# Performance work log

Hardware: AMD Instinct MI355X
Metric: run time of the kernel (lower is better)

## Reference

```python
import jax, jax.numpy as jnp
import numpy as np

N = 50000          # nodes
E = 800000         # directed edges (before self-loops)
F_IN = 256
HIDS = 32
HEADS = 8
N_CLASSES = 40
NEG_SLOPE = 0.2    # PyG GATConv default leaky_relu slope


def setup_inputs() -> dict:
    key = jax.random.key(0)
    ks = jax.random.split(key, 10)
    x = jax.random.normal(ks[0], (N, F_IN), dtype=jnp.float32)
    edge_index = jax.random.randint(ks[1], (2, E), 0, N, dtype=jnp.int32)
    # conv1: F_IN -> HIDS per head, HEADS heads, concat=True
    W1 = jax.random.normal(ks[2], (F_IN, HEADS * HIDS), dtype=jnp.float32) * (1.0 / np.sqrt(F_IN))
    a1_src = jax.random.normal(ks[3], (HEADS, HIDS), dtype=jnp.float32) * 0.1
    a1_dst = jax.random.normal(ks[4], (HEADS, HIDS), dtype=jnp.float32) * 0.1
    b1 = jnp.zeros((HEADS * HIDS,), dtype=jnp.float32)
    # conv2: HEADS*HIDS -> N_CLASSES, 1 head, concat=False
    W2 = jax.random.normal(ks[5], (HEADS * HIDS, N_CLASSES), dtype=jnp.float32) * (1.0 / np.sqrt(HEADS * HIDS))
    a2_src = jax.random.normal(ks[6], (1, N_CLASSES), dtype=jnp.float32) * 0.1
    a2_dst = jax.random.normal(ks[7], (1, N_CLASSES), dtype=jnp.float32) * 0.1
    b2 = jnp.zeros((N_CLASSES,), dtype=jnp.float32)
    return {"x": x, "edge_index": edge_index, "W1": W1, "a1_src": a1_src,
            "a1_dst": a1_dst, "b1": b1, "W2": W2, "a2_src": a2_src,
            "a2_dst": a2_dst, "b2": b2}


def _gat_conv(x, src, dst, W, a_src, a_dst, bias, heads, concat):
    n = x.shape[0]
    c = W.shape[1] // heads
    xw = (x @ W).reshape(n, heads, c)                       # [N,H,C]
    alpha_s = jnp.einsum('nhc,hc->nh', xw, a_src)           # [N,H]
    alpha_d = jnp.einsum('nhc,hc->nh', xw, a_dst)
    e = alpha_s[src] + alpha_d[dst]                         # [Etot,H]
    e = jnp.where(e >= 0, e, NEG_SLOPE * e)                 # leaky_relu
    # segment softmax over incoming edges of each destination node
    m = jax.ops.segment_max(e, dst, num_segments=n)         # [N,H]
    ex = jnp.exp(e - m[dst])
    denom = jax.ops.segment_sum(ex, dst, num_segments=n)    # [N,H]
    alpha = ex / denom[dst]                                 # [Etot,H]
    out = jax.ops.segment_sum(alpha[:, :, None] * xw[src], dst, num_segments=n)  # [N,H,C]
    if concat:
        out = out.reshape(n, heads * c)
    else:
        out = out.mean(axis=1)
    return out + bias


def reference(x, edge_index, W1, a1_src, a1_dst, b1, W2, a2_src, a2_dst, b2):
    n = x.shape[0]
    # add self-loops (PyG GATConv default)
    loop = jnp.arange(n, dtype=edge_index.dtype)
    src = jnp.concatenate([edge_index[0], loop])
    dst = jnp.concatenate([edge_index[1], loop])
    # dropout(p=0.6) layers are identity in eval mode
    h = _gat_conv(x, src, dst, W1, a1_src, a1_dst, b1, HEADS, True)
    h = jax.nn.elu(h)
    out = _gat_conv(h, src, dst, W2, a2_src, a2_dst, b2, 1, False)
    return out
```

## Files before the change

kernel.cpp:

```cpp
#include <hip/hip_runtime.h>
#include <hip/hip_bf16.h>

#define NNODES 50000
#define NPAD   50048
#define NEDGES 800000
#define ETOT   (NEDGES + NNODES)
#define FIN    256
#define HIDS   32
#define HEADS  8
#define NCLS   40
#define NEG    0.2f

#define SCAN_B 256
#define NSCB   ((NNODES + SCAN_B - 1) / SCAN_B)
#define NTILE1 ((NNODES + 63) / 64)

typedef __attribute__((ext_vector_type(8))) short bf16x8;
typedef __attribute__((ext_vector_type(4))) float f32x4;

__device__ __forceinline__ ushort f2bf(float f) {
  unsigned u = __float_as_uint(f);
  unsigned r = (u + 0x7fffu + ((u >> 16) & 1u)) >> 16;
  return (ushort)r;
}
__device__ __forceinline__ float bf2f(ushort u) {
  return __uint_as_float(((unsigned)u) << 16);
}
__device__ __forceinline__ float bflo(unsigned u) { return __uint_as_float(u << 16); }
__device__ __forceinline__ float bfhi(unsigned u) { return __uint_as_float(u & 0xffff0000u); }

__global__ __launch_bounds__(256) void prep_k(
    const float* __restrict__ W1, const float* __restrict__ W2,
    const float* __restrict__ a1src, const float* __restrict__ a1dst,
    const float* __restrict__ a2src, const float* __restrict__ a2dst,
    ushort* __restrict__ w1t, ushort* __restrict__ w2t,
    int* __restrict__ cnt, ushort* __restrict__ hb) {
  int b = blockIdx.x, t = threadIdx.x;
  if (b < 256) {
    int k = b, n = t;
    w1t[(size_t)n * 256 + k] = f2bf(W1[(size_t)k * 256 + n]);
  } else if (b < 272) {
    int j = b - 256, k = t;
    const float* av = (j < 8) ? (a1src + j * 32) : (a1dst + (j - 8) * 32);
    int nb = (j < 8) ? j * 32 : (j - 8) * 32;
    float s = 0.f;
#pragma unroll
    for (int c = 0; c < 32; ++c) s += W1[(size_t)k * 256 + nb + c] * av[c];
    w1t[(size_t)(256 + j) * 256 + k] = f2bf(s);
  } else if (b < 320) {
    w1t[(size_t)b * 256 + t] = 0;
  } else if (b < 384) {
    int n = b - 320, k = t;
    ushort v;
    if (n < NCLS) {
      v = f2bf(W2[(size_t)k * NCLS + n]);
    } else if (n == 40) {
      float s = 0.f;
#pragma unroll
      for (int c = 0; c < NCLS; ++c) s += W2[(size_t)k * NCLS + c] * a2src[c];
      v = f2bf(s);
    } else if (n == 41) {
      float s = 0.f;
#pragma unroll
      for (int c = 0; c < NCLS; ++c) s += W2[(size_t)k * NCLS + c] * a2dst[c];
      v = f2bf(s);
    } else {
      v = 0;
    }
    w2t[(size_t)n * 256 + k] = v;
  } else if (b < 580) {
    int i = (b - 384) * 256 + t;
    if (i < NNODES) cnt[i] = 0;
  } else {
    int r = NNODES + (b - 580);
    hb[(size_t)r * 256 + t] = 0;
  }
}

__global__ __launch_bounds__(256) void gemm1_mfma(
    const float* __restrict__ x, const ushort* __restrict__ w1t,
    ushort* __restrict__ xw1s, float* __restrict__ a1s, float* __restrict__ a1d) {
  __shared__ ushort As[64 * 40];
  __shared__ ushort Bs[320 * 40];
  const int tid = threadIdx.x;
  const int m0 = blockIdx.x * 64;
  const int w = tid >> 6, l = tid & 63, lr = l & 15, lq = l >> 4;
  f32x4 acc[4][5];
#pragma unroll
  for (int i = 0; i < 4; ++i)
#pragma unroll
    for (int j = 0; j < 5; ++j) acc[i][j] = (f32x4)0.f;

  for (int k0 = 0; k0 < 256; k0 += 32) {
    {
      int row = tid >> 2, kg = (tid & 3) * 8;
      int gr = m0 + row;
      bf16x8 av;
      if (gr < NNODES) {
        const float4* xp = (const float4*)(x + (size_t)gr * 256 + k0 + kg);
        float4 p0 = xp[0], p1 = xp[1];
        av[0] = (short)f2bf(p0.x); av[1] = (short)f2bf(p0.y);
        av[2] = (short)f2bf(p0.z); av[3] = (short)f2bf(p0.w);
        av[4] = (short)f2bf(p1.x); av[5] = (short)f2bf(p1.y);
        av[6] = (short)f2bf(p1.z); av[7] = (short)f2bf(p1.w);
      } else {
        av = (bf16x8)0;
      }
      *(bf16x8*)&As[row * 40 + kg] = av;
    }
#pragma unroll
    for (int p = 0; p < 5; ++p) {
      int idx = tid + p * 256;
      int n = idx >> 2, kg = (idx & 3) * 8;
      *(bf16x8*)&Bs[n * 40 + kg] = *(const bf16x8*)(w1t + (size_t)n * 256 + k0 + kg);
    }
    __syncthreads();
    bf16x8 af[4], bfr[5];
#pragma unroll
    for (int mt = 0; mt < 4; ++mt)
      af[mt] = *(const bf16x8*)&As[(mt * 16 + lr) * 40 + lq * 8];
#pragma unroll
    for (int nt = 0; nt < 5; ++nt) {
      int tile = nt * 4 + w;
      bfr[nt] = *(const bf16x8*)&Bs[(tile * 16 + lr) * 40 + lq * 8];
    }
#pragma unroll
    for (int mt = 0; mt < 4; ++mt)
#pragma unroll
      for (int nt = 0; nt < 5; ++nt)
        acc[mt][nt] = __builtin_amdgcn_mfma_f32_16x16x32_bf16(af[mt], bfr[nt], acc[mt][nt], 0, 0, 0);
    __syncthreads();
  }
#pragma unroll
  for (int mt = 0; mt < 4; ++mt)
#pragma unroll
    for (int nt = 0; nt < 5; ++nt) {
      int tile = nt * 4 + w;
      if (tile < 16) {
        int colc = tile * 16 + lr;
        int s = colc >> 5, c = colc & 31;
#pragma unroll
        for (int r = 0; r < 4; ++r) {
          int row = m0 + mt * 16 + lq * 4 + r;
          xw1s[((size_t)s * NPAD + row) * 32 + c] = f2bf(acc[mt][nt][r]);
        }
      } else if (tile == 16) {
#pragma unroll
        for (int r = 0; r < 4; ++r) {
          int row = m0 + mt * 16 + lq * 4 + r;
          if (lr < 8) a1s[(size_t)row * 8 + lr] = acc[mt][nt][r];
          else        a1d[(size_t)row * 8 + (lr - 8)] = acc[mt][nt][r];
        }
      }
    }
}

__global__ __launch_bounds__(256) void gemm2_mfma(
    const ushort* __restrict__ hb, const ushort* __restrict__ w2t,
    ushort* __restrict__ xw2b, float* __restrict__ a2s, float* __restrict__ a2d) {
  const int tid = threadIdx.x;
  const int w = tid >> 6, l = tid & 63, lr = l & 15, lq = l >> 4;
  const int row0 = blockIdx.x * 64 + w * 16;
  f32x4 acc[3];
#pragma unroll
  for (int i = 0; i < 3; ++i) acc[i] = (f32x4)0.f;
#pragma unroll
  for (int ks = 0; ks < 8; ++ks) {
    int k0 = ks * 32;
    bf16x8 af = *(const bf16x8*)(hb + (size_t)(row0 + lr) * 256 + k0 + lq * 8);
#pragma unroll
    for (int nt = 0; nt < 3; ++nt) {
      bf16x8 bfr = *(const bf16x8*)(w2t + (size_t)(nt * 16 + lr) * 256 + k0 + lq * 8);
      acc[nt] = __builtin_amdgcn_mfma_f32_16x16x32_bf16(af, bfr, acc[nt], 0, 0, 0);
    }
  }
#pragma unroll
  for (int nt = 0; nt < 3; ++nt) {
    int colc = nt * 16 + lr;
#pragma unroll
    for (int r = 0; r < 4; ++r) {
      int row = row0 + lq * 4 + r;
      if (colc < NCLS)      xw2b[(size_t)row * 40 + colc] = f2bf(acc[nt][r]);
      else if (colc == 40)  a2s[row] = acc[nt][r];
      else if (colc == 41)  a2d[row] = acc[nt][r];
    }
  }
}

__global__ __launch_bounds__(256) void hist_k(const int* __restrict__ dstA, int* __restrict__ cnt) {
  int e = blockIdx.x * 256 + threadIdx.x;
  if (e >= ETOT) return;
  int d = (e < NEDGES) ? dstA[e] : (e - NEDGES);
  atomicAdd(&cnt[d], 1);
}

__global__ __launch_bounds__(SCAN_B) void scan1_k(const int* __restrict__ deg,
                                                  int* __restrict__ row_ptr,
                                                  int* __restrict__ bsum) {
  __shared__ int sm[SCAN_B];
  int b = blockIdx.x, t = threadIdx.x;
  int idx = b * SCAN_B + t;
  int v = (idx < NNODES) ? deg[idx] : 0;
  sm[t] = v;
  __syncthreads();
#pragma unroll
  for (int off = 1; off < SCAN_B; off <<= 1) {
    int u = (t >= off) ? sm[t - off] : 0;
    __syncthreads();
    sm[t] += u;
    __syncthreads();
  }
  if (idx < NNODES) row_ptr[idx + 1] = sm[t];
  if (t == SCAN_B - 1) bsum[b] = sm[t];
}

__global__ __launch_bounds__(256) void scan2_k(int* __restrict__ bsum) {
  __shared__ int sm[256];
  int t = threadIdx.x;
  sm[t] = (t < NSCB) ? bsum[t] : 0;
  __syncthreads();
#pragma unroll
  for (int off = 1; off < 256; off <<= 1) {
    int u = (t >= off) ? sm[t - off] : 0;
    __syncthreads();
    sm[t] += u;
    __syncthreads();
  }
  if (t < NSCB) bsum[t] = (t > 0) ? sm[t - 1] : 0;
}

__global__ __launch_bounds__(SCAN_B) void scan3_k(const int* __restrict__ bsum,
                                                  int* __restrict__ row_ptr) {
  int b = blockIdx.x, t = threadIdx.x;
  int idx = b * SCAN_B + t;
  if (idx < NNODES) row_ptr[idx + 1] += bsum[b];
  if (b == 0 && t == 0) row_ptr[0] = 0;
}

__global__ __launch_bounds__(256) void scatter_k(const int* __restrict__ srcA, const int* __restrict__ dstA,
                                                 const int* __restrict__ row_ptr, int* __restrict__ cnt,
                                                 int* __restrict__ col, int* __restrict__ edst) {
  int e = blockIdx.x * 256 + threadIdx.x;
  if (e >= ETOT) return;
  int s, d;
  if (e < NEDGES) { s = srcA[e]; d = dstA[e]; }
  else { s = d = e - NEDGES; }
  int old = atomicSub(&cnt[d], 1);
  int pos = row_ptr[d] + old - 1;
  col[pos] = s;
  edst[pos] = d;
}

__global__ __launch_bounds__(256) void ew_k(
    const float* __restrict__ a1s, const float* __restrict__ a1d,
    const int* __restrict__ col, const int* __restrict__ edst,
    float* __restrict__ ew) {
  int pos = blockIdx.x * 256 + threadIdx.x;
  if (pos >= ETOT) return;
  int src = col[pos], dst = edst[pos];
  const float4* sp = (const float4*)(a1s + (size_t)src * 8);
  const float4* dp = (const float4*)(a1d + (size_t)dst * 8);
  float4 s0 = sp[0], s1 = sp[1];
  float4 d0 = dp[0], d1 = dp[1];
  float e[8] = {s0.x + d0.x, s0.y + d0.y, s0.z + d0.z, s0.w + d0.w,
                s1.x + d1.x, s1.y + d1.y, s1.z + d1.z, s1.w + d1.w};
#pragma unroll
  for (int h = 0; h < 8; ++h) {
    float v = e[h];
    v = fmaxf(v, 0.f) + NEG * fminf(v, 0.f);
    ew[(size_t)h * ETOT + pos] = __expf(v);
  }
}

__global__ __launch_bounds__(256) void agg1_k(
    const ushort* __restrict__ xw1s, const float* __restrict__ ew,
    const int* __restrict__ row_ptr, const int* __restrict__ col,
    const float* __restrict__ b1, ushort* __restrict__ hb) {
  const int b = blockIdx.x;
  const int s = b & 7;
  const int t = threadIdx.x;
  const int node = (b >> 3) * 64 + (t >> 2);
  const int q = t & 3;
  if (node >= NNODES) return;
  const ushort* xs = xw1s + (size_t)s * NPAD * 32 + q * 8;
  const float* ws = ew + (size_t)s * ETOT;
  int i = row_ptr[node];
  const int end = row_ptr[node + 1];
  float den = 0.f;
  float c0 = 0.f, c1 = 0.f, c2 = 0.f, c3 = 0.f, c4 = 0.f, c5 = 0.f, c6 = 0.f, c7 = 0.f;
  for (; i + 4 <= end; i += 4) {
    int s0 = col[i], s1 = col[i + 1], s2 = col[i + 2], s3 = col[i + 3];
    float w0 = ws[i], w1 = ws[i + 1], w2 = ws[i + 2], w3 = ws[i + 3];
    uint4 u0 = *(const uint4*)(xs + (size_t)s0 * 32);
    uint4 u1 = *(const uint4*)(xs + (size_t)s1 * 32);
    uint4 u2 = *(const uint4*)(xs + (size_t)s2 * 32);
    uint4 u3 = *(const uint4*)(xs + (size_t)s3 * 32);
    den += (w0 + w1) + (w2 + w3);
    c0 += w0 * bflo(u0.x) + w1 * bflo(u1.x) + w2 * bflo(u2.x) + w3 * bflo(u3.x);
    c1 += w0 * bfhi(u0.x) + w1 * bfhi(u1.x) + w2 * bfhi(u2.x) + w3 * bfhi(u3.x);
    c2 += w0 * bflo(u0.y) + w1 * bflo(u1.y) + w2 * bflo(u2.y) + w3 * bflo(u3.y);
    c3 += w0 * bfhi(u0.y) + w1 * bfhi(u1.y) + w2 * bfhi(u2.y) + w3 * bfhi(u3.y);
    c4 += w0 * bflo(u0.z) + w1 * bflo(u1.z) + w2 * bflo(u2.z) + w3 * bflo(u3.z);
    c5 += w0 * bfhi(u0.z) + w1 * bfhi(u1.z) + w2 * bfhi(u2.z) + w3 * bfhi(u3.z);
    c6 += w0 * bflo(u0.w) + w1 * bflo(u1.w) + w2 * bflo(u2.w) + w3 * bflo(u3.w);
    c7 += w0 * bfhi(u0.w) + w1 * bfhi(u1.w) + w2 * bfhi(u2.w) + w3 * bfhi(u3.w);
  }
  for (; i < end; ++i) {
    int s0 = col[i];
    float w0 = ws[i];
    uint4 u0 = *(const uint4*)(xs + (size_t)s0 * 32);
    den += w0;
    c0 += w0 * bflo(u0.x); c1 += w0 * bfhi(u0.x);
    c2 += w0 * bflo(u0.y); c3 += w0 * bfhi(u0.y);
    c4 += w0 * bflo(u0.z); c5 += w0 * bfhi(u0.z);
    c6 += w0 * bflo(u0.w); c7 += w0 * bfhi(u0.w);
  }
  const float inv = 1.f / den;
  const float4 bv0 = *reinterpret_cast<const float4*>(b1 + s * 32 + q * 8);
  const float4 bv1 = *reinterpret_cast<const float4*>(b1 + s * 32 + q * 8 + 4);
  float o[8];
  o[0] = c0 * inv + bv0.x; o[1] = c1 * inv + bv0.y;
  o[2] = c2 * inv + bv0.z; o[3] = c3 * inv + bv0.w;
  o[4] = c4 * inv + bv1.x; o[5] = c5 * inv + bv1.y;
  o[6] = c6 * inv + bv1.z; o[7] = c7 * inv + bv1.w;
  uint4 pk;
  unsigned r[4];
#pragma unroll
  for (int p = 0; p < 4; ++p) {
    float a = o[2 * p],     va = (a > 0.f) ? a : expm1f(a);
    float c = o[2 * p + 1], vc = (c > 0.f) ? c : expm1f(c);
    r[p] = (unsigned)f2bf(va) | ((unsigned)f2bf(vc) << 16);
  }
  pk.x = r[0]; pk.y = r[1]; pk.z = r[2]; pk.w = r[3];
  *(uint4*)(hb + (size_t)node * 256 + s * 32 + q * 8) = pk;
}

__global__ __launch_bounds__(256) void agg2_k(
    const ushort* __restrict__ xw2b, const float* __restrict__ a2s, const float* __restrict__ a2d,
    const int* __restrict__ row_ptr, const int* __restrict__ col,
    const float* __restrict__ b2, float* __restrict__ out, int n) {
  int wid = (blockIdx.x * 256 + threadIdx.x) >> 6;
  if (wid >= n) return;
  int lane = threadIdx.x & 63;
  int beg = row_ptr[wid], end = row_ptr[wid + 1];
  float ad = a2d[wid];
  float denom = 0.f, acc = 0.f;
  int i = beg;
  for (; i + 4 <= end; i += 4) {
    int s0 = col[i], s1 = col[i + 1], s2 = col[i + 2], s3 = col[i + 3];
    float e0 = a2s[s0] + ad;
    float e1 = a2s[s1] + ad;
    float e2 = a2s[s2] + ad;
    float e3 = a2s[s3] + ad;
    float w0 = __expf(fmaxf(e0, 0.f) + NEG * fminf(e0, 0.f));
    float w1 = __expf(fmaxf(e1, 0.f) + NEG * fminf(e1, 0.f));
    float w2 = __expf(fmaxf(e2, 0.f) + NEG * fminf(e2, 0.f));
    float w3 = __expf(fmaxf(e3, 0.f) + NEG * fminf(e3, 0.f));
    float x0 = 0.f, x1 = 0.f, x2 = 0.f, x3 = 0.f;
    if (lane < NCLS) {
      x0 = bf2f(xw2b[(size_t)s0 * 40 + lane]);
      x1 = bf2f(xw2b[(size_t)s1 * 40 + lane]);
      x2 = bf2f(xw2b[(size_t)s2 * 40 + lane]);
      x3 = bf2f(xw2b[(size_t)s3 * 40 + lane]);
    }
    denom += (w0 + w1) + (w2 + w3);
    acc += w0 * x0 + w1 * x1 + w2 * x2 + w3 * x3;
  }
  for (; i < end; ++i) {
    int s = col[i];
    float e = a2s[s] + ad;
    float w = __expf(fmaxf(e, 0.f) + NEG * fminf(e, 0.f));
    denom += w;
    if (lane < NCLS) acc += w * bf2f(xw2b[(size_t)s * 40 + lane]);
  }
  if (lane < NCLS) out[(size_t)wid * 40 + lane] = acc / denom + b2[lane];
}

extern "C" void kernel_launch(void* const* d_in, const int* in_sizes, int n_in,
                              void* d_out, int out_size, void* d_ws, size_t ws_size,
                              hipStream_t stream) {
  const float* x     = (const float*)d_in[0];
  const int*   ei    = (const int*)d_in[1];
  const float* W1    = (const float*)d_in[2];
  const float* a1src = (const float*)d_in[3];
  const float* a1dst = (const float*)d_in[4];
  const float* b1    = (const float*)d_in[5];
  const float* W2    = (const float*)d_in[6];
  const float* a2src = (const float*)d_in[7];
  const float* a2dst = (const float*)d_in[8];
  const float* b2    = (const float*)d_in[9];
  float* out = (float*)d_out;

  const int* srcA = ei;
  const int* dstA = ei + NEDGES;

  ushort* w1t  = (ushort*)d_ws;
  ushort* w2t  = w1t + (size_t)320 * 256;
  ushort* xw1s = w2t + (size_t)64 * 256;
  ushort* hb   = xw1s + (size_t)NPAD * 256;
  ushort* xw2b = hb + (size_t)NPAD * 256;
  float* a1s   = (float*)(xw2b + (size_t)NPAD * 40);
  float* a1d   = a1s + (size_t)NPAD * 8;
  float* a2s   = a1d + (size_t)NPAD * 8;
  float* a2d   = a2s + NPAD;
  float* ew    = a2d + NPAD;
  int* row_ptr = (int*)(ew + (size_t)8 * ETOT);
  int* cnt     = row_ptr + (NNODES + 1);
  int* col     = cnt + NNODES;
  int* edst    = col + ETOT;
  int* bsum    = edst + ETOT;

  prep_k<<<628, 256, 0, stream>>>(W1, W2, a1src, a1dst, a2src, a2dst, w1t, w2t, cnt, hb);

  gemm1_mfma<<<NPAD / 64, 256, 0, stream>>>(x, w1t, xw1s, a1s, a1d);

  hist_k<<<(ETOT + 255) / 256, 256, 0, stream>>>(dstA, cnt);
  scan1_k<<<NSCB, SCAN_B, 0, stream>>>(cnt, row_ptr, bsum);
  scan2_k<<<1, 256, 0, stream>>>(bsum);
  scan3_k<<<NSCB, SCAN_B, 0, stream>>>(bsum, row_ptr);
  scatter_k<<<(ETOT + 255) / 256, 256, 0, stream>>>(srcA, dstA, row_ptr, cnt, col, edst);

  ew_k<<<(ETOT + 255) / 256, 256, 0, stream>>>(a1s, a1d, col, edst, ew);

  agg1_k<<<NTILE1 * 8, 256, 0, stream>>>(xw1s, ew, row_ptr, col, b1, hb);

  gemm2_mfma<<<NPAD / 64, 256, 0, stream>>>(hb, w2t, xw2b, a2s, a2d);

  agg2_k<<<(NNODES + 3) / 4, 256, 0, stream>>>(xw2b, a2s, a2d, row_ptr, col, b2, out, NNODES);
}
```

Measured before the change: 263.8 us.

## Precompute layer-2 edge weights and remap agg2 to one lane per node

Adds an ew2_k kernel that computes the exponentiated layer-2 attention logits per CSR edge, so the aggregation no longer gathers a2s or evaluates exp per edge. agg2 changes from one 64-lane wave per node, with 24 lanes idle, to one lane per node, where each of 5 waves in a 320-thread block covers 8 classes using 16-byte bf16 loads. This mirrors the agg1 layout. It costs an extra launch and an extra 3.4 MB write and read. Lanes in a wave now walk different row lengths, so divergence and uncoalesced column and weight reads may appear.

```diff
diff --git a/kernel.cpp b/kernel.cpp
--- a/kernel.cpp
+++ b/kernel.cpp
@@ -270,6 +270,17 @@
     v = fmaxf(v, 0.f) + NEG * fminf(v, 0.f);
     ew[(size_t)h * ETOT + pos] = __expf(v);
   }
+}
+
+__global__ __launch_bounds__(256) void ew2_k(
+    const float* __restrict__ a2s, const float* __restrict__ a2d,
+    const int* __restrict__ col, const int* __restrict__ edst,
+    float* __restrict__ ew2) {
+  int pos = blockIdx.x * 256 + threadIdx.x;
+  if (pos >= ETOT) return;
+  float e = a2s[col[pos]] + a2d[edst[pos]];
+  e = fmaxf(e, 0.f) + NEG * fminf(e, 0.f);
+  ew2[pos] = __expf(e);
 }
 
 __global__ __launch_bounds__(256) void agg1_k(
@@ -335,45 +346,57 @@
   *(uint4*)(hb + (size_t)node * 256 + s * 32 + q * 8) = pk;
 }
 
-__global__ __launch_bounds__(256) void agg2_k(
-    const ushort* __restrict__ xw2b, const float* __restrict__ a2s, const float* __restrict__ a2d,
+__global__ __launch_bounds__(320) void agg2_k(
+    const ushort* __restrict__ xw2b, const float* __restrict__ ew2,
     const int* __restrict__ row_ptr, const int* __restrict__ col,
-    const float* __restrict__ b2, float* __restrict__ out, int n) {
-  int wid = (blockIdx.x * 256 + threadIdx.x) >> 6;
-  if (wid >= n) return;
-  int lane = threadIdx.x & 63;
-  int beg = row_ptr[wid], end = row_ptr[wid + 1];
-  float ad = a2d[wid];
-  float denom = 0.f, acc = 0.f;
-  int i = beg;
+    const float* __restrict__ b2, float* __restrict__ out) {
+  const int t = threadIdx.x;
+  const int lane = t & 63;
+  const int g = t >> 6;
+  const int node = blockIdx.x * 64 + lane;
+  if (node >= NNODES) return;
+  const int c0off = g * 8;
+  int i = row_ptr[node];
+  const int end = row_ptr[node + 1];
+  float den = 0.f;
+  float c0 = 0.f, c1 = 0.f, c2 = 0.f, c3 = 0.f, c4 = 0.f, c5 = 0.f, c6 = 0.f, c7 = 0.f;
   for (; i + 4 <= end; i += 4) {
     int s0 = col[i], s1 = col[i + 1], s2 = col[i + 2], s3 = col[i + 3];
-    float e0 = a2s[s0] + ad;
-    float e1 = a2s[s1] + ad;
-    float e2 = a2s[s2] + ad;
-    float e3 = a2s[s3] + ad;
-    float w0 = __expf(fmaxf(e0, 0.f) + NEG * fminf(e0, 0.f));
-    float w1 = __expf(fmaxf(e1, 0.f) + NEG * fminf(e1, 0.f));
-    float w2 = __expf(fmaxf(e2, 0.f) + NEG * fminf(e2, 0.f));
-    float w3 = __expf(fmaxf(e3, 0.f) + NEG * fminf(e3, 0.f));
-    float x0 = 0.f, x1 = 0.f, x2 = 0.f, x3 = 0.f;
-    if (lane < NCLS) {
-      x0 = bf2f(xw2b[(size_t)s0 * 40 + lane]);
-      x1 = bf2f(xw2b[(size_t)s1 * 40 + lane]);
-      x2 = bf2f(xw2b[(size_t)s2 * 40 + lane]);
-      x3 = bf2f(xw2b[(size_t)s3 * 40 + lane]);
-    }
-    denom += (w0 + w1) + (w2 + w3);
-    acc += w0 * x0 + w1 * x1 + w2 * x2 + w3 * x3;
+    float w0 = ew2[i], w1 = ew2[i + 1], w2 = ew2[i + 2], w3 = ew2[i + 3];
+    uint4 u0 = *(const uint4*)(xw2b + (size_t)s0 * 40 + c0off);
+    uint4 u1 = *(const uint4*)(xw2b + (size_t)s1 * 40 + c0off);
+    uint4 u2 = *(const uint4*)(xw2b + (size_t)s2 * 40 + c0off);
+    uint4 u3 = *(const uint4*)(xw2b + (size_t)s3 * 40 + c0off);
+    den += (w0 + w1) + (w2 + w3);
+    c0 += w0 * bflo(u0.x) + w1 * bflo(u1.x) + w2 * bflo(u2.x) + w3 * bflo(u3.x);
+    c1 += w0 * bfhi(u0.x) + w1 * bfhi(u1.x) + w2 * bfhi(u2.x) + w3 * bfhi(u3.x);
+    c2 += w0 * bflo(u0.y) + w1 * bflo(u1.y) + w2 * bflo(u2.y) + w3 * bflo(u3.y);
+    c3 += w0 * bfhi(u0.y) + w1 * bfhi(u1.y) + w2 * bfhi(u2.y) + w3 * bfhi(u3.y);
+    c4 += w0 * bflo(u0.z) + w1 * bflo(u1.z) + w2 * bflo(u2.z) + w3 * bflo(u3.z);
+    c5 += w0 * bfhi(u0.z) + w1 * bfhi(u1.z) + w2 * bfhi(u2.z) + w3 * bfhi(u3.z);
+    c6 += w0 * bflo(u0.w) + w1 * bflo(u1.w) + w2 * bflo(u2.w) + w3 * bflo(u3.w);
+    c7 += w0 * bfhi(u0.w) + w1 * bfhi(u1.w) + w2 * bfhi(u2.w) + w3 * bfhi(u3.w);
   }
   for (; i < end; ++i) {
-    int s = col[i];
-    float e = a2s[s] + ad;
-    float w = __expf(fmaxf(e, 0.f) + NEG * fminf(e, 0.f));
-    denom += w;
-    if (lane < NCLS) acc += w * bf2f(xw2b[(size_t)s * 40 + lane]);
-  }
-  if (lane < NCLS) out[(size_t)wid * 40 + lane] = acc / denom + b2[lane];
+    int s0 = col[i];
+    float w0 = ew2[i];
+    uint4 u0 = *(const uint4*)(xw2b + (size_t)s0 * 40 + c0off);
+    den += w0;
+    c0 += w0 * bflo(u0.x); c1 += w0 * bfhi(u0.x);
+    c2 += w0 * bflo(u0.y); c3 += w0 * bfhi(u0.y);
+    c4 += w0 * bflo(u0.z); c5 += w0 * bfhi(u0.z);
+    c6 += w0 * bflo(u0.w); c7 += w0 * bfhi(u0.w);
+  }
+  const float inv = 1.f / den;
+  const float* bp = b2 + c0off;
+  float o[8];
+  o[0] = c0 * inv + bp[0]; o[1] = c1 * inv + bp[1];
+  o[2] = c2 * inv + bp[2]; o[3] = c3 * inv + bp[3];
+  o[4] = c4 * inv + bp[4]; o[5] = c5 * inv + bp[5];
+  o[6] = c6 * inv + bp[6]; o[7] = c7 * inv + bp[7];
+  float* op = out + (size_t)node * 40 + c0off;
+  *(float4*)op = make_float4(o[0], o[1], o[2], o[3]);
+  *(float4*)(op + 4) = make_float4(o[4], o[5], o[6], o[7]);
 }
 
 extern "C" void kernel_launch(void* const* d_in, const int* in_sizes, int n_in,
@@ -404,7 +427,8 @@
   float* a2s   = a1d + (size_t)NPAD * 8;
   float* a2d   = a2s + NPAD;
   float* ew    = a2d + NPAD;
-  int* row_ptr = (int*)(ew + (size_t)8 * ETOT);
+  float* ew2   = ew + (size_t)8 * ETOT;
+  int* row_ptr = (int*)(ew2 + ETOT);
   int* cnt     = row_ptr + (NNODES + 1);
   int* col     = cnt + NNODES;
   int* edst    = col + ETOT;
@@ -426,5 +450,7 @@
 
   gemm2_mfma<<<NPAD / 64, 256, 0, stream>>>(hb, w2t, xw2b, a2s, a2d);
 
-  agg2_k<<<(NNODES + 3) / 4, 256, 0, stream>>>(xw2b, a2s, a2d, row_ptr, col, b2, out, NNODES);
-}
+  ew2_k<<<(ETOT + 255) / 256, 256, 0, stream>>>(a2s, a2d, col, edst, ew2);
+
+  agg2_k<<<NTILE1, 320, 0, stream>>>(xw2b, ew2, row_ptr, col, b2, out);
+}
```

Result: no change. 264.5 us (+0.3%).
